# Kernel optimization log

Measured on AMD Instinct MI355X. Metric: run time of the kernel, lower is better.

## Reference

```python
import jax, jax.numpy as jnp
import numpy as np

B, S, E, H = 4, 2048, 1024, 16
D = E // H


def setup_inputs() -> dict:
    key = jax.random.key(0)
    ks = jax.random.split(key, 6)
    scale = 1.0 / np.sqrt(E).astype(np.float32)
    return {
        "x": jax.random.normal(ks[0], (B, S, E), jnp.float32),
        # positive entries -> cumsum normalizer is well conditioned
        "weight": jax.random.uniform(ks[1], (H, S), jnp.float32, 0.05, 1.0),
        "bias": jax.random.normal(ks[2], (H, S), jnp.float32) * 0.02,
        "inp_w": jax.random.normal(ks[3], (E, E), jnp.float32) * scale,
        "inp_b": jax.random.normal(ks[4], (E,), jnp.float32) * 0.02,
        "out_w": jax.random.normal(ks[5], (E, E), jnp.float32) * scale,
    }


def reference(x, weight, bias, inp_w, inp_b, out_w):
    Bx, Sx, Ex = x.shape
    Hx = weight.shape[0]
    Dx = Ex // Hx
    # input projection (torch Linear: x @ W.T + b)
    x = x @ inp_w.T + inp_b
    # (B,S,E) -> (B,E,S) -> (B,H,D,S)
    xh = x.transpose(0, 2, 1).reshape(Bx, Hx, Dx, Sx)
    # Toeplitz causal matrix per head: M[h,i,j] = weight[h, j-i] if j>=i else 0
    idx = jnp.arange(Sx)
    off = idx[None, :] - idx[:, None]  # (S,S)
    M = jnp.where(off >= 0, weight[:, off], jnp.zeros((), x.dtype))  # (H,S,S)
    # batched matmul over the sequence axis: y[b,h,d,t] = sum_s x[b,h,d,s] M[h,s,t]
    y = jnp.einsum('bhds,hst->bhdt', xh, M)
    # cumulative-sum normalization (do_toep_mean=True)
    norm = jnp.cumsum(weight, axis=-1)  # (H,S)
    y = y / norm[None, :, None, :]
    # per-head, per-position bias
    y = y + bias[None, :, None, :]
    # (B,H,D,S) -> (B,E,S) -> (B,S,E)
    y = y.reshape(Bx, Ex, Sx).transpose(0, 2, 1)
    # output projection (no bias)
    return y @ out_w.T
```

## Files before the change

### kernel.cpp

```cpp
#include <hip/hip_runtime.h>

typedef unsigned short u16;
typedef __attribute__((ext_vector_type(4))) float f32x4;
typedef __attribute__((ext_vector_type(8))) __bf16 bf16x8;

__device__ __forceinline__ u16 f2bf(float f) {
  unsigned u = __builtin_bit_cast(unsigned, f);
  u = u + 0x7fffu + ((u >> 16) & 1u);
  return (u16)(u >> 16);
}

__device__ __forceinline__ void load_lds16(const void* g, void* l) {
  __builtin_amdgcn_global_load_lds((__attribute__((address_space(1))) void*)g,
                                   (__attribute__((address_space(3))) void*)l,
                                   16, 0, 0);
}

__device__ __forceinline__ f32x4 MF(bf16x8 a, bf16x8 b, f32x4 c) {
  return __builtin_amdgcn_mfma_f32_16x16x32_bf16(a, b, c, 0, 0, 0);
}

#define VROWS 2176

__global__ __launch_bounds__(256) void prep_all(const float* __restrict__ x,
                                                const float* __restrict__ inp_w,
                                                const float* __restrict__ out_w,
                                                const float* __restrict__ weight,
                                                u16* __restrict__ Xb,
                                                u16* __restrict__ Wb,
                                                u16* __restrict__ OWb,
                                                float* __restrict__ normB,
                                                u16* __restrict__ V) {
  const int bx = blockIdx.x, tid = threadIdx.x;
  if (bx < 10240) {
    const float* src; u16* dst; int i;
    if (bx < 8192)      { src = x;     dst = Xb;  i = bx * 256 + tid; }
    else if (bx < 9216) { src = inp_w; dst = Wb;  i = (bx - 8192) * 256 + tid; }
    else                { src = out_w; dst = OWb; i = (bx - 9216) * 256 + tid; }
    const float4 v = ((const float4*)src)[i];
    ushort4 o;
    o.x = f2bf(v.x); o.y = f2bf(v.y); o.z = f2bf(v.z); o.w = f2bf(v.w);
    ((ushort4*)dst)[i] = o;
    return;
  }
  if (bx < 10256) {
    const int h = bx - 10240;
    __shared__ float ts[256];
    float v[8];
    const float* src = weight + h * 2048 + tid * 8;
    float s = 0.f;
#pragma unroll
    for (int j = 0; j < 8; ++j) v[j] = src[j];
#pragma unroll
    for (int j = 0; j < 8; ++j) { s += v[j]; v[j] = s; }
    ts[tid] = s;
    __syncthreads();
    float xx = s;
#pragma unroll
    for (int d = 1; d < 256; d <<= 1) {
      float y = (tid >= d) ? ts[tid - d] : 0.f;
      __syncthreads();
      xx += y;
      ts[tid] = xx;
      __syncthreads();
    }
    const float excl = xx - s;
    float* dst = normB + h * 2048 + tid * 8;
#pragma unroll
    for (int j = 0; j < 8; ++j) dst[j] = excl + v[j];
    return;
  }
  if (bx < 10512) {
    const int bb = bx - 10256;
    const int h = bb & 15, tb = bb >> 4;
    __shared__ u16 wl[2048];
#pragma unroll
    for (int j = 0; j < 8; ++j) wl[tid * 8 + j] = f2bf(weight[h * 2048 + tid * 8 + j]);
    __syncthreads();
#pragma unroll
    for (int i = 0; i < 8; ++i) {
      const int cid = i * 256 + tid;
      const int row = cid >> 4, c = cid & 15;
      const int t = tb * 128 + row;
      const int j0 = c * 8;
      unsigned v[8];
#pragma unroll
      for (int jj = 0; jj < 8; ++jj) {
        const int j = j0 + jj;
        v[jj] = (t >= j) ? (unsigned)wl[t - j] : 0u;
      }
      uint4 o;
      o.x = v[0] | (v[1] << 16); o.y = v[2] | (v[3] << 16);
      o.z = v[4] | (v[5] << 16); o.w = v[6] | (v[7] << 16);
      *(uint4*)(V + ((size_t)h * VROWS + 128 + t) * 128 + j0) = o;
    }
    return;
  }
  {
    const int bb = bx - 10512;
    const int h = bb >> 1, part = bb & 1;
    uint4 z; z.x = z.y = z.z = z.w = 0u;
    uint4* dst = (uint4*)(V + (size_t)h * VROWS * 128 + part * 8192) + tid * 4;
#pragma unroll
    for (int j = 0; j < 4; ++j) dst[j] = z;
  }
}

template <bool BIAS, bool F32OUT, int DEC>
__global__ __launch_bounds__(256) void gemm_nt4(const u16* __restrict__ A,
                                                const u16* __restrict__ B,
                                                void* __restrict__ C,
                                                const float* __restrict__ bias,
                                                int K, int lda, int ldb, int ldc) {
  __shared__ __align__(16) u16 As[2][128 * 64];
  __shared__ __align__(16) u16 Bs[2][128 * 64];
  const int tid = threadIdx.x;
  const int lane = tid & 63, wv = tid >> 6;
  const int wm = wv >> 1, wn = wv & 1;
  const int l15 = lane & 15, g = lane >> 4;

  const int flat = (int)blockIdx.x;
  int m0, n0;
  if (DEC == 0) {
    const int xcd = flat & 7, i = flat >> 3;
    m0 = (i & 7) * 128;
    n0 = ((xcd << 3) + (i >> 3)) * 128;
  } else {
    const int sw = (flat & 7) * 64 + (flat >> 3);
    m0 = (sw >> 3) * 128;
    n0 = (sw & 7) * 128;
  }

  const int NT = K >> 6;

  auto stage = [&](int t, int bi) {
    const int kt = t << 6;
#pragma unroll
    for (int i = 0; i < 4; ++i) {
      const int c = i * 256 + tid;
      const int row = c >> 3, cc = c & 7;
      load_lds16(A + (size_t)(m0 + row) * lda + kt + ((cc ^ (row & 7)) << 3),
                 &As[bi][i * 2048 + wv * 512]);
    }
#pragma unroll
    for (int i = 0; i < 4; ++i) {
      const int c = i * 256 + tid;
      const int row = c >> 3, cc = c & 7;
      load_lds16(B + (size_t)(n0 + row) * ldb + kt + ((cc ^ (row & 7)) << 3),
                 &Bs[bi][i * 2048 + wv * 512]);
    }
  };

  f32x4 acc[4][4] = {};
  stage(0, 0);
  __syncthreads();
  int cur = 0;
  for (int t = 0; t < NT; ++t) {
    if (t + 1 < NT) stage(t + 1, cur ^ 1);
#pragma unroll
    for (int kh = 0; kh < 2; ++kh) {
      bf16x8 af[4], bf[4];
#pragma unroll
      for (int mf = 0; mf < 4; ++mf) {
        const int row = wm * 64 + mf * 16 + l15;
        af[mf] = *(const bf16x8*)(&As[cur][row * 64 + ((((kh << 2) + g) ^ (row & 7)) << 3)]);
      }
#pragma unroll
      for (int nf = 0; nf < 4; ++nf) {
        const int row = wn * 64 + nf * 16 + l15;
        bf[nf] = *(const bf16x8*)(&Bs[cur][row * 64 + ((((kh << 2) + g) ^ (row & 7)) << 3)]);
      }
      __builtin_amdgcn_s_setprio(1);
#pragma unroll
      for (int mf = 0; mf < 4; ++mf)
#pragma unroll
        for (int nf = 0; nf < 4; ++nf)
          acc[mf][nf] = MF(af[mf], bf[nf], acc[mf][nf]);
      __builtin_amdgcn_s_setprio(0);
    }
    __syncthreads();
    cur ^= 1;
  }

#pragma unroll
  for (int mf = 0; mf < 4; ++mf) {
#pragma unroll
    for (int r = 0; r < 4; ++r) {
      const int row = m0 + wm * 64 + mf * 16 + g * 4 + r;
      const float bb = BIAS ? bias[row] : 0.f;
#pragma unroll
      for (int nf = 0; nf < 4; ++nf) {
        const int col = n0 + wn * 64 + nf * 16 + l15;
        const float v = acc[mf][nf][r] + bb;
        if (F32OUT)
          ((float*)C)[(size_t)row * ldc + col] = v;
        else
          ((u16*)C)[(size_t)row * ldc + col] = f2bf(v);
      }
    }
  }
}

__global__ __launch_bounds__(256) void toep_conv(const u16* __restrict__ X1t,
                                                 const u16* __restrict__ Vpad,
                                                 const float* __restrict__ normB,
                                                 const float* __restrict__ biasB,
                                                 u16* __restrict__ Y2b) {
  __shared__ __align__(16) u16 As[2][256 * 64];
  __shared__ __align__(16) u16 Xs[2][64 * 64];
  const int tid = threadIdx.x;
  const int lane = tid & 63, wv = tid >> 6;
  const int l15 = lane & 15, g = lane >> 4;

  const int x = (int)blockIdx.x;
  const int h = (x & 7) + 8 * ((x >> 3) & 1);
  const int rest = x >> 4;
  const int tb = 7 - (rest & 7);
  const int b = rest >> 3;

  const int t0 = tb * 256;
  const int Q = 4 * tb + 4;

  const u16* Vbase = Vpad + (size_t)h * VROWS * 128 + (size_t)(128 + t0) * 128;
  const u16* Xrow = X1t + (size_t)h * 64 * 8192 + b * 2048;

  auto stage = [&](int q, int bi) {
    const int st = q >> 1, half = q & 1;
    const u16* Ab = Vbase - (size_t)st * 128 * 128 + half * 64;
#pragma unroll
    for (int i = 0; i < 8; ++i) {
      const int c = i * 256 + tid;
      const int row = c >> 3, cc = c & 7;
      load_lds16(Ab + (size_t)row * 128 + ((cc ^ (row & 7)) << 3),
                 &As[bi][i * 2048 + wv * 512]);
    }
    const int s0 = q * 64;
#pragma unroll
    for (int i = 0; i < 2; ++i) {
      const int c = i * 256 + tid;
      const int row = c >> 3, cc = c & 7;
      load_lds16(Xrow + (size_t)row * 8192 + s0 + ((cc ^ (row & 7)) << 3),
                 &Xs[bi][i * 2048 + wv * 512]);
    }
  };

  f32x4 acc[4][4] = {};
  stage(0, 0);
  __syncthreads();
  int cur = 0;
  for (int q = 0; q < Q; ++q) {
    if (q + 1 < Q) stage(q + 1, cur ^ 1);
#pragma unroll
    for (int ks = 0; ks < 2; ++ks) {
      bf16x8 af[4], bv[4];
#pragma unroll
      for (int tf = 0; tf < 4; ++tf) {
        const int trow = wv * 64 + tf * 16 + l15;
        af[tf] = *(const bf16x8*)(&As[cur][trow * 64 + ((((ks << 2) + g) ^ (trow & 7)) << 3)]);
      }
#pragma unroll
      for (int nf = 0; nf < 4; ++nf) {
        const int drow = nf * 16 + l15;
        bv[nf] = *(const bf16x8*)(&Xs[cur][drow * 64 + ((((ks << 2) + g) ^ (drow & 7)) << 3)]);
      }
      __builtin_amdgcn_s_setprio(1);
#pragma unroll
      for (int tf = 0; tf < 4; ++tf)
#pragma unroll
        for (int nf = 0; nf < 4; ++nf)
          acc[tf][nf] = MF(af[tf], bv[nf], acc[tf][nf]);
      __builtin_amdgcn_s_setprio(0);
    }
    __syncthreads();
    cur ^= 1;
  }

#pragma unroll
  for (int tf = 0; tf < 4; ++tf) {
#pragma unroll
    for (int r = 0; r < 4; ++r) {
      const int t = t0 + wv * 64 + tf * 16 + g * 4 + r;
      const float inv = 1.0f / normB[h * 2048 + t];
      const float bb = biasB[h * 2048 + t];
#pragma unroll
      for (int nf = 0; nf < 4; ++nf) {
        const int d = nf * 16 + l15;
        Y2b[(size_t)(b * 2048 + t) * 1024 + h * 64 + d] = f2bf(acc[tf][nf][r] * inv + bb);
      }
    }
  }
}

extern "C" void kernel_launch(void* const* d_in, const int* in_sizes, int n_in,
                              void* d_out, int out_size, void* d_ws, size_t ws_size,
                              hipStream_t stream) {
  (void)in_sizes; (void)n_in; (void)out_size; (void)ws_size;
  const float* x      = (const float*)d_in[0];
  const float* weight = (const float*)d_in[1];
  const float* biasB  = (const float*)d_in[2];
  const float* inp_w  = (const float*)d_in[3];
  const float* inp_b  = (const float*)d_in[4];
  const float* out_w  = (const float*)d_in[5];

  char* ws = (char*)d_ws;
  u16* Xb    = (u16*)(ws + 0);
  u16* X1t   = (u16*)(ws + (size_t)(16u << 20));
  u16* Y2b   = (u16*)(ws + (size_t)(32u << 20));
  u16* Wb    = (u16*)(ws + (size_t)(48u << 20));
  u16* OWb   = (u16*)(ws + (size_t)(50u << 20));
  float* normB = (float*)(ws + (size_t)(52u << 20));
  u16* Vt    = (u16*)(ws + (size_t)(53u << 20));

  prep_all<<<10544, 256, 0, stream>>>(x, inp_w, out_w, weight, Xb, Wb, OWb, normB, Vt);

  gemm_nt4<true, false, 0><<<512, 256, 0, stream>>>(
      Wb, Xb, (void*)X1t, inp_b, 1024, 1024, 1024, 8192);

  toep_conv<<<512, 256, 0, stream>>>(X1t, Vt, normB, biasB, Y2b);

  gemm_nt4<false, true, 1><<<512, 256, 0, stream>>>(
      Y2b, OWb, d_out, nullptr, 1024, 1024, 1024, 1024);
}
```

Before: 106.1 us.

## Pair causal tiles per block and triple-buffer toeplitz conv loads

The Toeplitz conv kernel now launches 256 blocks, and each block handles two time tiles (tb = 7-p and p) so that every block does the same total amount of causal work. This removes the triangular load imbalance. The LDS double buffer becomes a triple buffer with prefetch distance two, and explicit vmcnt waits plus raw s_barrier replace __syncthreads, so global loads overlap more MFMA work. The cost is more LDS per block (about 120KB), which limits occupancy, and half as many blocks to fill the CUs.

```diff
diff --git a/kernel.cpp b/kernel.cpp
--- a/kernel.cpp
+++ b/kernel.cpp
@@ -206,8 +206,8 @@
                                                  const float* __restrict__ normB,
                                                  const float* __restrict__ biasB,
                                                  u16* __restrict__ Y2b) {
-  __shared__ __align__(16) u16 As[2][256 * 64];
-  __shared__ __align__(16) u16 Xs[2][64 * 64];
+  __shared__ __align__(16) u16 As[3][256 * 64];
+  __shared__ __align__(16) u16 Xs[3][64 * 64];
   const int tid = threadIdx.x;
   const int lane = tid & 63, wv = tid >> 6;
   const int l15 = lane & 15, g = lane >> 4;
@@ -215,77 +215,91 @@
   const int x = (int)blockIdx.x;
   const int h = (x & 7) + 8 * ((x >> 3) & 1);
   const int rest = x >> 4;
-  const int tb = 7 - (rest & 7);
-  const int b = rest >> 3;
-
-  const int t0 = tb * 256;
-  const int Q = 4 * tb + 4;
-
-  const u16* Vbase = Vpad + (size_t)h * VROWS * 128 + (size_t)(128 + t0) * 128;
+  const int p = rest & 3, b = rest >> 2;
+
+  const u16* Vh = Vpad + (size_t)h * VROWS * 128;
   const u16* Xrow = X1t + (size_t)h * 64 * 8192 + b * 2048;
 
-  auto stage = [&](int q, int bi) {
-    const int st = q >> 1, half = q & 1;
-    const u16* Ab = Vbase - (size_t)st * 128 * 128 + half * 64;
-#pragma unroll
-    for (int i = 0; i < 8; ++i) {
-      const int c = i * 256 + tid;
-      const int row = c >> 3, cc = c & 7;
-      load_lds16(Ab + (size_t)row * 128 + ((cc ^ (row & 7)) << 3),
-                 &As[bi][i * 2048 + wv * 512]);
-    }
-    const int s0 = q * 64;
-#pragma unroll
-    for (int i = 0; i < 2; ++i) {
-      const int c = i * 256 + tid;
-      const int row = c >> 3, cc = c & 7;
-      load_lds16(Xrow + (size_t)row * 8192 + s0 + ((cc ^ (row & 7)) << 3),
-                 &Xs[bi][i * 2048 + wv * 512]);
-    }
-  };
-
-  f32x4 acc[4][4] = {};
-  stage(0, 0);
-  __syncthreads();
-  int cur = 0;
-  for (int q = 0; q < Q; ++q) {
-    if (q + 1 < Q) stage(q + 1, cur ^ 1);
-#pragma unroll
-    for (int ks = 0; ks < 2; ++ks) {
-      bf16x8 af[4], bv[4];
-#pragma unroll
-      for (int tf = 0; tf < 4; ++tf) {
-        const int trow = wv * 64 + tf * 16 + l15;
-        af[tf] = *(const bf16x8*)(&As[cur][trow * 64 + ((((ks << 2) + g) ^ (trow & 7)) << 3)]);
-      }
-#pragma unroll
-      for (int nf = 0; nf < 4; ++nf) {
-        const int drow = nf * 16 + l15;
-        bv[nf] = *(const bf16x8*)(&Xs[cur][drow * 64 + ((((ks << 2) + g) ^ (drow & 7)) << 3)]);
-      }
-      __builtin_amdgcn_s_setprio(1);
-#pragma unroll
-      for (int tf = 0; tf < 4; ++tf)
-#pragma unroll
-        for (int nf = 0; nf < 4; ++nf)
-          acc[tf][nf] = MF(af[tf], bv[nf], acc[tf][nf]);
-      __builtin_amdgcn_s_setprio(0);
-    }
-    __syncthreads();
-    cur ^= 1;
-  }
-
-#pragma unroll
-  for (int tf = 0; tf < 4; ++tf) {
-#pragma unroll
-    for (int r = 0; r < 4; ++r) {
-      const int t = t0 + wv * 64 + tf * 16 + g * 4 + r;
-      const float inv = 1.0f / normB[h * 2048 + t];
-      const float bb = biasB[h * 2048 + t];
-#pragma unroll
-      for (int nf = 0; nf < 4; ++nf) {
-        const int d = nf * 16 + l15;
-        Y2b[(size_t)(b * 2048 + t) * 1024 + h * 64 + d] = f2bf(acc[tf][nf][r] * inv + bb);
+#pragma unroll 1
+  for (int ti = 0; ti < 2; ++ti) {
+    const int tt = ti ? p : 7 - p;
+    const int t0 = tt * 256;
+    const int Q = 4 * tt + 4;
+    const u16* Vbase = Vh + (size_t)(128 + t0) * 128;
+
+    auto stage = [&](int q, int bi) {
+      const int st = q >> 1, half = q & 1;
+      const u16* Ab = Vbase - (size_t)st * 128 * 128 + half * 64;
+#pragma unroll
+      for (int i = 0; i < 8; ++i) {
+        const int c = i * 256 + tid;
+        const int row = c >> 3, cc = c & 7;
+        load_lds16(Ab + (size_t)row * 128 + ((cc ^ (row & 7)) << 3),
+                   &As[bi][i * 2048 + wv * 512]);
+      }
+      const int s0 = q * 64;
+#pragma unroll
+      for (int i = 0; i < 2; ++i) {
+        const int c = i * 256 + tid;
+        const int row = c >> 3, cc = c & 7;
+        load_lds16(Xrow + (size_t)row * 8192 + s0 + ((cc ^ (row & 7)) << 3),
+                   &Xs[bi][i * 2048 + wv * 512]);
+      }
+    };
+
+    f32x4 acc[4][4] = {};
+    stage(0, 0);
+    stage(1, 1);
+    asm volatile("s_waitcnt vmcnt(10)" ::: "memory");
+    __builtin_amdgcn_sched_barrier(0);
+    __builtin_amdgcn_s_barrier();
+    asm volatile("" ::: "memory");
+
+    int cur = 0;
+#pragma unroll 1
+    for (int q = 0; q < Q; ++q) {
+      if (q + 2 < Q) stage(q + 2, (q + 2) % 3);
+#pragma unroll
+      for (int ks = 0; ks < 2; ++ks) {
+        bf16x8 af[4], bv[4];
+#pragma unroll
+        for (int tf = 0; tf < 4; ++tf) {
+          const int trow = wv * 64 + tf * 16 + l15;
+          af[tf] = *(const bf16x8*)(&As[cur][trow * 64 + ((((ks << 2) + g) ^ (trow & 7)) << 3)]);
+        }
+#pragma unroll
+        for (int nf = 0; nf < 4; ++nf) {
+          const int drow = nf * 16 + l15;
+          bv[nf] = *(const bf16x8*)(&Xs[cur][drow * 64 + ((((ks << 2) + g) ^ (drow & 7)) << 3)]);
+        }
+        __builtin_amdgcn_s_setprio(1);
+#pragma unroll
+        for (int tf = 0; tf < 4; ++tf)
+#pragma unroll
+          for (int nf = 0; nf < 4; ++nf)
+            acc[tf][nf] = MF(af[tf], bv[nf], acc[tf][nf]);
+        __builtin_amdgcn_s_setprio(0);
+      }
+      if (q + 2 < Q)      asm volatile("s_waitcnt vmcnt(10)" ::: "memory");
+      else if (q + 1 < Q) asm volatile("s_waitcnt vmcnt(0)" ::: "memory");
+      __builtin_amdgcn_sched_barrier(0);
+      __builtin_amdgcn_s_barrier();
+      asm volatile("" ::: "memory");
+      cur = (cur == 2) ? 0 : cur + 1;
+    }
+
+#pragma unroll
+    for (int tf = 0; tf < 4; ++tf) {
+#pragma unroll
+      for (int r = 0; r < 4; ++r) {
+        const int t = t0 + wv * 64 + tf * 16 + g * 4 + r;
+        const float inv = 1.0f / normB[h * 2048 + t];
+        const float bb = biasB[h * 2048 + t];
+#pragma unroll
+        for (int nf = 0; nf < 4; ++nf) {
+          const int d = nf * 16 + l15;
+          Y2b[(size_t)(b * 2048 + t) * 1024 + h * 64 + d] = f2bf(acc[tf][nf][r] * inv + bb);
+        }
       }
     }
   }
@@ -316,7 +330,7 @@
   gemm_nt4<true, false, 0><<<512, 256, 0, stream>>>(
       Wb, Xb, (void*)X1t, inp_b, 1024, 1024, 1024, 8192);
 
-  toep_conv<<<512, 256, 0, stream>>>(X1t, Vt, normB, biasB, Y2b);
+  toep_conv<<<256, 256, 0, stream>>>(X1t, Vt, normB, biasB, Y2b);
 
   gemm_nt4<false, true, 1><<<512, 256, 0, stream>>>(
       Y2b, OWb, d_out, nullptr, 1024, 1024, 1024, 1024);
```

After: 106.9 us. No clear change (+0.7%).

## Load Toeplitz operand directly to registers and widen conv blocks to 512 threads

Applied to the files above, without the earlier changes.

The Toeplitz convolution kernel no longer stages the 256x64 Toeplitz tile through LDS. Each wave now loads its A fragments straight from global memory into registers. Only the small X tile stays double-buffered in LDS, synchronised with raw barriers and hand-placed vmcnt waits. The block grows to 8 waves of 32 rows each, and block-to-tile mapping alternates direction so long and short causal rows interleave. This cuts LDS footprint and LDS write/read traffic, at the cost of uncoalesced 16-byte global loads, fragile manual waitcnt counting, and more register-level latency exposure.

```diff
diff --git a/kernel.cpp b/kernel.cpp
--- a/kernel.cpp
+++ b/kernel.cpp
@@ -201,12 +201,11 @@
   }
 }
 
-__global__ __launch_bounds__(256) void toep_conv(const u16* __restrict__ X1t,
+__global__ __launch_bounds__(512) void toep_conv(const u16* __restrict__ X1t,
                                                  const u16* __restrict__ Vpad,
                                                  const float* __restrict__ normB,
                                                  const float* __restrict__ biasB,
                                                  u16* __restrict__ Y2b) {
-  __shared__ __align__(16) u16 As[2][256 * 64];
   __shared__ __align__(16) u16 Xs[2][64 * 64];
   const int tid = threadIdx.x;
   const int lane = tid & 63, wv = tid >> 6;
@@ -214,72 +213,72 @@
 
   const int x = (int)blockIdx.x;
   const int h = (x & 7) + 8 * ((x >> 3) & 1);
-  const int rest = x >> 4;
-  const int tb = 7 - (rest & 7);
-  const int b = rest >> 3;
-
+  const int t0raw = (x >> 4) & 7;
+  const int b = (x >> 7) & 3;
+  const int tb = ((x >> 8) & 1) ? 7 - t0raw : t0raw;
   const int t0 = tb * 256;
   const int Q = 4 * tb + 4;
 
-  const u16* Vbase = Vpad + (size_t)h * VROWS * 128 + (size_t)(128 + t0) * 128;
+  const u16* Vh = Vpad + (size_t)h * VROWS * 128;
   const u16* Xrow = X1t + (size_t)h * 64 * 8192 + b * 2048;
 
-  auto stage = [&](int q, int bi) {
+  const int srow = tid >> 3, scc = tid & 7;
+  const u16* Xsrc = Xrow + (size_t)srow * 8192 + ((scc ^ (srow & 7)) << 3);
+
+  f32x4 acc[2][4] = {};
+  load_lds16(Xsrc + 0, &Xs[0][wv * 512]);
+
+#pragma unroll 1
+  for (int q = 0; q < Q; ++q) {
+    const bool pf = (q + 1 < Q);
+    __builtin_amdgcn_s_barrier();
+    if (pf) load_lds16(Xsrc + (q + 1) * 64, &Xs[(q + 1) & 1][wv * 512]);
+
     const int st = q >> 1, half = q & 1;
-    const u16* Ab = Vbase - (size_t)st * 128 * 128 + half * 64;
-#pragma unroll
-    for (int i = 0; i < 8; ++i) {
-      const int c = i * 256 + tid;
-      const int row = c >> 3, cc = c & 7;
-      load_lds16(Ab + (size_t)row * 128 + ((cc ^ (row & 7)) << 3),
-                 &As[bi][i * 2048 + wv * 512]);
-    }
-    const int s0 = q * 64;
-#pragma unroll
-    for (int i = 0; i < 2; ++i) {
-      const int c = i * 256 + tid;
-      const int row = c >> 3, cc = c & 7;
-      load_lds16(Xrow + (size_t)row * 8192 + s0 + ((cc ^ (row & 7)) << 3),
-                 &Xs[bi][i * 2048 + wv * 512]);
-    }
-  };
-
-  f32x4 acc[4][4] = {};
-  stage(0, 0);
-  __syncthreads();
-  int cur = 0;
-  for (int q = 0; q < Q; ++q) {
-    if (q + 1 < Q) stage(q + 1, cur ^ 1);
-#pragma unroll
-    for (int ks = 0; ks < 2; ++ks) {
-      bf16x8 af[4], bv[4];
-#pragma unroll
-      for (int tf = 0; tf < 4; ++tf) {
-        const int trow = wv * 64 + tf * 16 + l15;
-        af[tf] = *(const bf16x8*)(&As[cur][trow * 64 + ((((ks << 2) + g) ^ (trow & 7)) << 3)]);
-      }
+    const u16* Ab = Vh + (size_t)(128 + t0 - st * 128) * 128 + half * 64;
+    bf16x8 af00, af01, af10, af11;
+    {
+      const int trow0 = wv * 32 + l15;
+      const int trow1 = trow0 + 16;
+      const u16* r0 = Ab + (size_t)trow0 * 128 + g * 8;
+      const u16* r1 = Ab + (size_t)trow1 * 128 + g * 8;
+      af00 = *(const bf16x8*)(r0);
+      af01 = *(const bf16x8*)(r0 + 32);
+      af10 = *(const bf16x8*)(r1);
+      af11 = *(const bf16x8*)(r1 + 32);
+    }
+    asm volatile("" : "+v"(af00), "+v"(af01), "+v"(af10), "+v"(af11));
+    if (pf) asm volatile("s_waitcnt vmcnt(5)" ::: "memory");
+    else    asm volatile("s_waitcnt vmcnt(4)" ::: "memory");
+    __builtin_amdgcn_sched_barrier(0);
+    __builtin_amdgcn_s_barrier();
+    __builtin_amdgcn_sched_barrier(0);
+
+#pragma unroll
+    for (int kh = 0; kh < 2; ++kh) {
+      bf16x8 bv[4];
 #pragma unroll
       for (int nf = 0; nf < 4; ++nf) {
         const int drow = nf * 16 + l15;
-        bv[nf] = *(const bf16x8*)(&Xs[cur][drow * 64 + ((((ks << 2) + g) ^ (drow & 7)) << 3)]);
-      }
+        bv[nf] = *(const bf16x8*)(&Xs[q & 1][drow * 64 + ((((kh << 2) + g) ^ (drow & 7)) << 3)]);
+      }
+      const bf16x8 a0 = kh ? af01 : af00;
+      const bf16x8 a1 = kh ? af11 : af10;
       __builtin_amdgcn_s_setprio(1);
 #pragma unroll
-      for (int tf = 0; tf < 4; ++tf)
-#pragma unroll
-        for (int nf = 0; nf < 4; ++nf)
-          acc[tf][nf] = MF(af[tf], bv[nf], acc[tf][nf]);
+      for (int nf = 0; nf < 4; ++nf) {
+        acc[0][nf] = MF(a0, bv[nf], acc[0][nf]);
+        acc[1][nf] = MF(a1, bv[nf], acc[1][nf]);
+      }
       __builtin_amdgcn_s_setprio(0);
     }
-    __syncthreads();
-    cur ^= 1;
-  }
-
-#pragma unroll
-  for (int tf = 0; tf < 4; ++tf) {
+  }
+
+#pragma unroll
+  for (int tf = 0; tf < 2; ++tf) {
 #pragma unroll
     for (int r = 0; r < 4; ++r) {
-      const int t = t0 + wv * 64 + tf * 16 + g * 4 + r;
+      const int t = t0 + wv * 32 + tf * 16 + g * 4 + r;
       const float inv = 1.0f / normB[h * 2048 + t];
       const float bb = biasB[h * 2048 + t];
 #pragma unroll
@@ -316,7 +315,7 @@
   gemm_nt4<true, false, 0><<<512, 256, 0, stream>>>(
       Wb, Xb, (void*)X1t, inp_b, 1024, 1024, 1024, 8192);
 
-  toep_conv<<<512, 256, 0, stream>>>(X1t, Vt, normB, biasB, Y2b);
+  toep_conv<<<512, 512, 0, stream>>>(X1t, Vt, normB, biasB, Y2b);
 
   gemm_nt4<false, true, 1><<<512, 256, 0, stream>>>(
       Y2b, OWb, d_out, nullptr, 1024, 1024, 1024, 1024);
```

Measured after the change: 121.5 us. +14.4%, slower.
